# Optimization experiments

Measured on AMD Instinct MI355X. Metric: run time of the kernel, lower is better.

Reference implementation:

```python
import jax, jax.numpy as jnp
import numpy as np

B, C, T, V = 64, 3, 300, 25   # V == time_serious
CC, TS, TL = 100, 25, 9        # causal_channel, time_serious, time_len


def _bn2d(h, g, b, eps=1e-5):
    # training-mode BatchNorm2d: biased batch stats over (B, T, V)
    mu = h.mean(axis=(0, 2, 3), keepdims=True)
    var = h.var(axis=(0, 2, 3), keepdims=True)
    return g[None, :, None, None] * (h - mu) / jnp.sqrt(var + eps) + b[None, :, None, None]


def setup_inputs() -> dict:
    key = jax.random.key(0)
    ks = jax.random.split(key, 32)
    s = 0.1
    weight = jax.random.uniform(ks[1], (CC, TS, TL), minval=-0.163, maxval=0.163)  # ~kaiming_uniform fan_in=225
    inp = {
        'x': jax.random.normal(ks[0], (B, C, T, V)),
        'weight': weight,
        'weight_norm': jnp.linalg.norm(weight, axis=0),  # frozen at init, detached buffer
        'fb0_w': jax.random.normal(ks[2], (64, 3)) * s,
        'fb0_b': jax.random.normal(ks[3], (64,)) * s,
        'bn0_g': jnp.ones((64,)), 'bn0_b': jnp.zeros((64,)),
        'fb1_w': jax.random.normal(ks[4], (128, 64)) * s,
        'fb1_b': jax.random.normal(ks[5], (128,)) * s,
        'bn1_g': jnp.ones((128,)), 'bn1_b': jnp.zeros((128,)),
        'fb2_w': jax.random.normal(ks[6], (1, 128)) * s,
        'fb2_b': jax.random.normal(ks[7], (1,)) * s,
        'bn2_g': jnp.ones((1,)), 'bn2_b': jnp.zeros((1,)),
        'c1_w': jax.random.normal(ks[8], (CC, 1)) * s,
        'c1_b': jax.random.normal(ks[9], (CC,)) * s,
        'c2_w': jax.random.normal(ks[10], (CC, 1)) * s,
        'c2_b': jax.random.normal(ks[11], (CC,)) * s,
        'f0_w': jax.random.normal(ks[12], (TS, 100, 100)) * s,
        'f0_b': jax.random.normal(ks[13], (TS, 100)) * s,
        'f1_w': jax.random.normal(ks[14], (TS, 10, 100)) * s,
        'f1_b': jax.random.normal(ks[15], (TS, 10)) * s,
        'f2_w': jax.random.normal(ks[16], (TS, 1, 10)) * s,
        'f2_b': jax.random.normal(ks[17], (TS, 1)) * s,
    }
    return inp


def reference(x, weight, weight_norm, fb0_w, fb0_b, bn0_g, bn0_b, fb1_w, fb1_b, bn1_g, bn1_b,
              fb2_w, fb2_b, bn2_g, bn2_b, c1_w, c1_b, c2_w, c2_b,
              f0_w, f0_b, f1_w, f1_b, f2_w, f2_b):
    Bx, Cx, Tx, Vx = x.shape
    CCx, TSx, TLx = weight.shape
    L = Tx - TLx + 1

    # feature_update branches: 1x1 conv2d -> BN -> ReLU
    h = x
    for w, bb, g, bt in ((fb0_w, fb0_b, bn0_g, bn0_b),
                         (fb1_w, fb1_b, bn1_g, bn1_b),
                         (fb2_w, fb2_b, bn2_g, bn2_b)):
        h = jnp.einsum('oc,bctv->botv', w, h) + bb[None, :, None, None]
        h = jax.nn.relu(_bn2d(h, g, bt))
    # h: [B, 1, T, V]

    x1 = (jnp.einsum('oc,bctv->botv', c1_w, h) + c1_b[None, :, None, None]).mean(axis=2)  # [B,CC,V]
    x2 = (jnp.einsum('oc,bctv->botv', c2_w, h) + c2_b[None, :, None, None]).mean(axis=2)  # [B,CC,V]
    cm = jnp.tanh(x1[:, :, :, None] - x2[:, :, None, :])  # causal_matrix [B,CC,V,V]

    x_series = jnp.transpose(h[:, 0], (0, 2, 1))  # [B,V,T]
    wn = weight / jax.lax.stop_gradient(weight_norm)[None]  # [CC,TS,TL]

    # fused equivalent of the per-i grouped conv1d loop:
    # ret_i[b,c,t] = sum_{v,l} x_series[b,v,t+l] * cm[b,c,v,i] * wn[c,v,l]
    windows = jnp.stack([x_series[:, :, l:l + L] for l in range(TLx)], axis=-1)  # [B,V,L,TL]
    Fc = jnp.einsum('bvtl,cvl->bcvt', windows, wn)       # [B,CC,V,L]
    p = jnp.einsum('bcvi,bcvt->bict', cm, Fc)            # [B,TS,CC,L] (i = stacked channel group)

    # follow_branches: grouped 1x1 conv1d (groups = TS) + ReLU
    for w, bb in ((f0_w, f0_b), (f1_w, f1_b), (f2_w, f2_b)):
        p = jax.nn.relu(jnp.einsum('goc,bgct->bgot', w, p) + bb[None, :, :, None])
    p = p[:, :, 0, :]  # [B,V,L]

    predic_loss = jnp.mean((x_series[:, :, TLx:] - p[:, :, :-1]) ** 2)

    # GSGL penalty on causal_matrix
    n1 = jnp.linalg.norm(cm, axis=1)  # [B,V,V]
    panelty = 1e-4 * (jnp.linalg.norm(n1, axis=1).sum() + n1.sum())

    regularize = 1e-4 * (jnp.sum(f0_w ** 2) + jnp.sum(f1_w ** 2) + jnp.sum(f2_w ** 2))

    # GC: norm over channel then lag of cm[...,None] * weight -> closed form
    GCs = jnp.sqrt(jnp.einsum('bcvm,cm->bvm', cm ** 2, jnp.sum(weight ** 2, axis=-1)))
    return (GCs, predic_loss, panelty, regularize)
```

## Files before the change

kernel.cpp:

```cpp
#include <hip/hip_runtime.h>
#include <hip/hip_bf16.h>
#include <string.h>

#define N_POS 480000
#define NB    64
#define NT    300
#define NV    25
#define NCC   100
#define NTL   9
#define NL    292

#define WS_XA     0
#define WS_Z2SUM  144
#define WS_Z2SQ   160
#define WS_LOSS   176
#define WS_PAN    192
#define WS_REG    208
#define WS_SC1    224
#define WS_SH1    352
#define WS_SC2    480
#define WS_SH2    481
#define WS_WA     512
#define WS_W1T    768
#define WS_SW     8960
#define WS_HM     11460
#define WS_Z1P    13060
#define WS_Z1PQ   77060
#define WS_Z2     141060
#define WS_XS     621060
#define WS_CM     1101060
#define WS_P      5101060

__device__ __forceinline__ float waveRed(float v) {
    #pragma unroll
    for (int off = 32; off > 0; off >>= 1) v += __shfl_down(v, off);
    return v;
}

__global__ __launch_bounds__(256) void k_xstats(const float* __restrict__ x,
                                                float* __restrict__ ws) {
    __shared__ float s_red[4][9];
    int tid = blockIdx.x * 256 + threadIdx.x;
    int nth = gridDim.x * 256;
    float a[9];
    #pragma unroll
    for (int i = 0; i < 9; i++) a[i] = 0.f;
    for (int task = tid; task < 120000; task += nth) {
        int b = task / 1875; int q = task - b*1875;
        const float* xb = x + b*22500 + q*4;
        float4 v0 = *(const float4*)(xb);
        float4 v1 = *(const float4*)(xb + 7500);
        float4 v2 = *(const float4*)(xb + 15000);
        const float* p0 = (const float*)&v0;
        const float* p1 = (const float*)&v1;
        const float* p2 = (const float*)&v2;
        #pragma unroll
        for (int k = 0; k < 4; k++) {
            float x0 = p0[k], x1 = p1[k], x2 = p2[k];
            a[0] += x0; a[1] += x1; a[2] += x2;
            a[3] = fmaf(x0,x0,a[3]); a[4] = fmaf(x0,x1,a[4]); a[5] = fmaf(x0,x2,a[5]);
            a[6] = fmaf(x1,x1,a[6]); a[7] = fmaf(x1,x2,a[7]); a[8] = fmaf(x2,x2,a[8]);
        }
    }
    #pragma unroll
    for (int i = 0; i < 9; i++) a[i] = waveRed(a[i]);
    int w = threadIdx.x >> 6;
    if ((threadIdx.x & 63) == 0) {
        #pragma unroll
        for (int i = 0; i < 9; i++) s_red[w][i] = a[i];
    }
    __syncthreads();
    if (threadIdx.x < 9) {
        float s = s_red[0][threadIdx.x] + s_red[1][threadIdx.x]
                + s_red[2][threadIdx.x] + s_red[3][threadIdx.x];
        atomicAdd(&ws[WS_XA + threadIdx.x*16], s);
    }
}

__global__ void k_prepw(const float* __restrict__ weight, float* __restrict__ ws) {
    int idx = blockIdx.x * blockDim.x + threadIdx.x;
    if (idx < 2500) {
        float s = 0;
        #pragma unroll
        for (int l = 0; l < NTL; l++) { float w = weight[idx*NTL + l]; s += w*w; }
        ws[WS_SW + idx] = s;
    }
}

__global__ void k_prepw1t(const float* __restrict__ w1g, float* __restrict__ ws) {
    int idx = blockIdx.x * 256 + threadIdx.x;
    if (idx < 8192) {
        int c = idx >> 7, o = idx & 127;
        ws[WS_W1T + idx] = w1g[o*64 + c];
    }
}

__global__ void k_prep0(const float* __restrict__ w, const float* __restrict__ bb,
                        const float* __restrict__ g, const float* __restrict__ bt,
                        float* __restrict__ ws) {
    int o = threadIdx.x;
    float inv = 1.0f / (float)N_POS;
    float mx0 = ws[WS_XA+0]*inv, mx1 = ws[WS_XA+16]*inv, mx2 = ws[WS_XA+32]*inv;
    float C00 = ws[WS_XA+48]*inv  - mx0*mx0;
    float C01 = ws[WS_XA+64]*inv  - mx0*mx1;
    float C02 = ws[WS_XA+80]*inv  - mx0*mx2;
    float C11 = ws[WS_XA+96]*inv  - mx1*mx1;
    float C12 = ws[WS_XA+112]*inv - mx1*mx2;
    float C22 = ws[WS_XA+128]*inv - mx2*mx2;
    float w0 = w[o*3], w1 = w[o*3+1], w2 = w[o*3+2];
    float mu  = w0*mx0 + w1*mx1 + w2*mx2 + bb[o];
    float var = w0*w0*C00 + w1*w1*C11 + w2*w2*C22
              + 2.f*(w0*w1*C01 + w0*w2*C02 + w1*w2*C12);
    float sc = g[o] / sqrtf(var + 1e-5f);
    float sh = bt[o] - sc*mu;
    ws[WS_WA + o*4 + 0] = sc*w0;
    ws[WS_WA + o*4 + 1] = sc*w1;
    ws[WS_WA + o*4 + 2] = sc*w2;
    ws[WS_WA + o*4 + 3] = sc*bb[o] + sh;
}

#define ZP_BLOCKS 500
#define ZP_CHUNKS 15
template<int MODE>
__global__ __launch_bounds__(256) void k_zpass(
        const float* __restrict__ x,
        const float* __restrict__ b1g,
        const float* __restrict__ w2g,
        const float* __restrict__ b2g,
        float* __restrict__ ws) {
    __shared__ float smem[12544];
    float* s_h0  = smem;
    float* s_w1t = smem + 4352;
    int tid = threadIdx.x;

    for (int i = tid; i < 8192; i += 256) s_w1t[i] = ws[WS_W1T + i];

    int pos = tid & 63, cset = tid >> 6;
    int pg  = tid >> 4, og  = tid & 15;

    float b1r[8];
    #pragma unroll
    for (int o = 0; o < 8; o++) b1r[o] = b1g[og*8 + o];
    float sc1r[8], sh1r[8], w2r[8], b2v = 0.f;
    if constexpr (MODE == 1) {
        #pragma unroll
        for (int o = 0; o < 8; o++) {
            sc1r[o] = ws[WS_SC1 + og*8 + o];
            sh1r[o] = ws[WS_SH1 + og*8 + o];
            w2r[o]  = w2g[og*8 + o];
        }
        b2v = b2g[0];
    }
    float zs[8], zq[8];
    #pragma unroll
    for (int o = 0; o < 8; o++) { zs[o] = 0.f; zq[o] = 0.f; }
    float z2s = 0.f, z2q = 0.f;

    __syncthreads();

    for (int ci = 0; ci < ZP_CHUNKS; ci++) {
        int chunk = blockIdx.x * ZP_CHUNKS + ci;
        int P = chunk*64 + pos;
        int b = P / 7500, rem = P - b*7500;
        const float* xb = x + b*22500 + rem;
        float x0 = xb[0], x1 = xb[7500], x2 = xb[15000];
        #pragma unroll
        for (int k = 0; k < 16; k++) {
            int ch = cset*16 + k;
            const float4 wa = *(const float4*)&ws[WS_WA + ch*4];
            s_h0[ch*68 + pos] = fmaxf(wa.x*x0 + wa.y*x1 + wa.z*x2 + wa.w, 0.f);
        }
        __syncthreads();

        float acc[4][8];
        #pragma unroll
        for (int p = 0; p < 4; p++)
            #pragma unroll
            for (int o = 0; o < 8; o++) acc[p][o] = 0.f;

        #pragma unroll 4
        for (int c = 0; c < 64; c++) {
            float4 ha = *(const float4*)&s_h0[c*68 + 4*pg];
            float4 wl = *(const float4*)&s_w1t[c*128 + 8*og];
            float4 wh = *(const float4*)&s_w1t[c*128 + 8*og + 4];
            #pragma unroll
            for (int p = 0; p < 4; p++) {
                float hv = ((const float*)&ha)[p];
                #pragma unroll
                for (int o = 0; o < 4; o++) {
                    acc[p][o]   = fmaf(hv, ((const float*)&wl)[o], acc[p][o]);
                    acc[p][o+4] = fmaf(hv, ((const float*)&wh)[o], acc[p][o+4]);
                }
            }
        }

        if constexpr (MODE == 0) {
            #pragma unroll
            for (int o = 0; o < 8; o++) {
                #pragma unroll
                for (int p = 0; p < 4; p++) {
                    float z = acc[p][o] + b1r[o];
                    zs[o] += z; zq[o] += z*z;
                }
            }
            __syncthreads();
        } else {
            float zp[4];
            #pragma unroll
            for (int p = 0; p < 4; p++) {
                float s = 0.f;
                #pragma unroll
                for (int o = 0; o < 8; o++) {
                    float z = acc[p][o] + b1r[o];
                    s += w2r[o]*fmaxf(sc1r[o]*z + sh1r[o], 0.f);
                }
                zp[p] = s;
            }
            __syncthreads();
            float* s_z2p = smem;
            #pragma unroll
            for (int p = 0; p < 4; p++) s_z2p[(4*pg + p)*17 + og] = zp[p];
            __syncthreads();
            if (tid < 64) {
                float z2 = b2v;
                #pragma unroll
                for (int j = 0; j < 16; j++) z2 += s_z2p[tid*17 + j];
                ws[WS_Z2 + chunk*64 + tid] = z2;
                z2s += z2; z2q += z2*z2;
            }
            __syncthreads();
        }
    }

    if constexpr (MODE == 0) {
        float* s_part = smem;
        #pragma unroll
        for (int o = 0; o < 8; o++) s_part[(og*8 + o)*17 + pg] = zs[o];
        __syncthreads();
        if (tid < 128) {
            float s = 0.f;
            #pragma unroll
            for (int j = 0; j < 16; j++) s += s_part[tid*17 + j];
            ws[WS_Z1P + blockIdx.x*128 + tid] = s;
        }
        __syncthreads();
        #pragma unroll
        for (int o = 0; o < 8; o++) s_part[(og*8 + o)*17 + pg] = zq[o];
        __syncthreads();
        if (tid < 128) {
            float s = 0.f;
            #pragma unroll
            for (int j = 0; j < 16; j++) s += s_part[tid*17 + j];
            ws[WS_Z1PQ + blockIdx.x*128 + tid] = s;
        }
    } else {
        if (tid < 64) {
            z2s = waveRed(z2s);
            z2q = waveRed(z2q);
            if (tid == 0) { atomicAdd(&ws[WS_Z2SUM], z2s); atomicAdd(&ws[WS_Z2SQ], z2q); }
        }
    }
}

__global__ __launch_bounds__(256) void k_z1red(const float* __restrict__ g,
                                               const float* __restrict__ bt,
                                               float* __restrict__ ws) {
    __shared__ float ss[4], qq[4];
    int o = blockIdx.x;
    float s = 0.f, q = 0.f;
    for (int blk = threadIdx.x; blk < ZP_BLOCKS; blk += 256) {
        s += ws[WS_Z1P  + blk*128 + o];
        q += ws[WS_Z1PQ + blk*128 + o];
    }
    s = waveRed(s); q = waveRed(q);
    int w = threadIdx.x >> 6;
    if ((threadIdx.x & 63) == 0) { ss[w] = s; qq[w] = q; }
    __syncthreads();
    if (threadIdx.x == 0) {
        float S = ss[0]+ss[1]+ss[2]+ss[3];
        float Q = qq[0]+qq[1]+qq[2]+qq[3];
        float inv = 1.0f / (float)N_POS;
        float m = S*inv;
        float v = Q*inv - m*m;
        float sc = g[o] / sqrtf(v + 1e-5f);
        ws[WS_SC1+o] = sc;
        ws[WS_SH1+o] = bt[o] - sc*m;
    }
}

__global__ void k_prep2(const float* __restrict__ g, const float* __restrict__ bt,
                        float* __restrict__ ws) {
    float inv = 1.0f / (float)N_POS;
    float m = ws[WS_Z2SUM]*inv;
    float v = ws[WS_Z2SQ]*inv - m*m;
    float sc = g[0] / sqrtf(v + 1e-5f);
    ws[WS_SC2] = sc;
    ws[WS_SH2] = bt[0] - sc*m;
}

__global__ void k_xs(float* __restrict__ ws) {
    __shared__ float red[128];
    int bid = blockIdx.x;
    int b = bid / 25, v = bid - b*25;
    float sc = ws[WS_SC2], sh = ws[WS_SH2];
    float local = 0.f;
    for (int t = threadIdx.x; t < NT; t += 128) {
        float val = fmaxf(sc * ws[WS_Z2 + b*7500 + t*25 + v] + sh, 0.f);
        ws[WS_XS + (size_t)bid*NT + t] = val;
        local += val;
    }
    red[threadIdx.x] = local;
    __syncthreads();
    for (int s = 64; s > 0; s >>= 1) {
        if (threadIdx.x < s) red[threadIdx.x] += red[threadIdx.x + s];
        __syncthreads();
    }
    if (threadIdx.x == 0) ws[WS_HM + bid] = red[0] * (1.f/300.f);
}

__global__ void k_cm(const float* __restrict__ c1w, const float* __restrict__ c1b,
                     const float* __restrict__ c2w, const float* __restrict__ c2b,
                     float* __restrict__ ws) {
    __shared__ float s_hm[25];
    int bid = blockIdx.x;
    int b = bid / 100, c = bid - b*100;
    if (threadIdx.x < 25) s_hm[threadIdx.x] = ws[WS_HM + b*25 + threadIdx.x];
    float a1 = c1w[c], d1 = c1b[c], a2 = c2w[c], d2 = c2b[c];
    __syncthreads();
    for (int idx = threadIdx.x; idx < 625; idx += 256) {
        int i = idx / 25, j = idx - i*25;
        ws[WS_CM + (size_t)bid*625 + idx] = tanhf(a1*s_hm[i] + d1 - a2*s_hm[j] - d2);
    }
}

__global__ void k_gcs(const float* __restrict__ ws, float* __restrict__ out) {
    int gid = blockIdx.x * 256 + threadIdx.x;
    if (gid < 40000) {
        int b = gid / 625; int rem = gid - b*625; int m = rem % 25;
        float acc = 0.f;
        for (int c = 0; c < 100; c++) {
            float v = ws[WS_CM + ((size_t)(b*100+c))*625 + rem];
            acc += v*v*ws[WS_SW + c*25 + m];
        }
        out[gid] = sqrtf(acc);
    }
}

__global__ void k_pan(float* __restrict__ ws) {
    __shared__ float s_colsq[25];
    __shared__ float s_n1, s_r;
    int tid = threadIdx.x;
    int b = blockIdx.x;
    if (tid < 25) s_colsq[tid] = 0.f;
    if (tid == 0) { s_n1 = 0.f; s_r = 0.f; }
    __syncthreads();
    float ln1 = 0.f;
    for (int idx = tid; idx < 625; idx += 256) {
        int j = idx % 25;
        float sq = 0.f;
        for (int c = 0; c < 100; c++) {
            float v = ws[WS_CM + ((size_t)(b*100+c))*625 + idx];
            sq += v*v;
        }
        ln1 += sqrtf(sq);
        atomicAdd(&s_colsq[j], sq);
    }
    ln1 = waveRed(ln1);
    if ((tid & 63) == 0) atomicAdd(&s_n1, ln1);
    __syncthreads();
    if (tid < 25) atomicAdd(&s_r, sqrtf(s_colsq[tid]));
    __syncthreads();
    if (tid == 0) atomicAdd(&ws[WS_PAN], s_n1 + s_r);
}

__global__ void k_reg(const float* __restrict__ f0w, const float* __restrict__ f1w,
                      const float* __restrict__ f2w, float* __restrict__ ws) {
    __shared__ float sred[4];
    int tid = blockIdx.x * blockDim.x + threadIdx.x;
    int nth = gridDim.x * blockDim.x;
    float a = 0.f;
    for (int i = tid; i < 275250; i += nth) {
        float w;
        if (i < 250000) w = f0w[i];
        else if (i < 275000) w = f1w[i - 250000];
        else w = f2w[i - 275000];
        a += w*w;
    }
    a = waveRed(a);
    int w = threadIdx.x >> 6;
    if ((threadIdx.x & 63) == 0) sred[w] = a;
    __syncthreads();
    if (threadIdx.x == 0)
        atomicAdd(&ws[WS_REG], sred[0]+sred[1]+sred[2]+sred[3]);
}

#define XP 156
#define FP 152
__global__ __launch_bounds__(256) void k_fcp(
        const float* __restrict__ weight, const float* __restrict__ wnorm,
        float* __restrict__ pbuf, const float* __restrict__ ws, int b_base) {
    __shared__ float s_xs[25*XP];
    __shared__ float s_fc[25*FP];
    __shared__ float s_wn[225];
    __shared__ float s_cm[625];
    int tid = threadIdx.x;
    int bid = blockIdx.x;
    int bl = bid / 100, c = bid - bl*100;
    int b = b_base + bl;

    for (int i = tid; i < 225; i += 256) s_wn[i] = weight[c*225 + i] / wnorm[i];
    for (int i = tid; i < 625; i += 256) s_cm[i] = ws[WS_CM + ((size_t)(b*100+c))*625 + i];

    #pragma unroll
    for (int h = 0; h < 2; h++) {
        const int t_base = h ? 148 : 0;
        const int TH     = h ? 144 : 148;
        const int NTQ4   = TH / 4;
        const int NPV    = ((TH + 7) / 8);

        for (int i = tid; i < 25*XP; i += 256) {
            int v = i / XP, u = i - v*XP;
            if (u < TH + 8) s_xs[i] = ws[WS_XS + (size_t)(b*25+v)*NT + t_base + u];
        }
        __syncthreads();

        for (int task = tid; task < 25*NTQ4; task += 256) {
            int v = task / NTQ4, tq = task - v*NTQ4;
            int t0 = tq*4;
            float4 xa = *(const float4*)&s_xs[v*XP + t0];
            float4 xb = *(const float4*)&s_xs[v*XP + t0 + 4];
            float4 xc = *(const float4*)&s_xs[v*XP + t0 + 8];
            float xr[12];
            xr[0]=xa.x; xr[1]=xa.y; xr[2]=xa.z; xr[3]=xa.w;
            xr[4]=xb.x; xr[5]=xb.y; xr[6]=xb.z; xr[7]=xb.w;
            xr[8]=xc.x; xr[9]=xc.y; xr[10]=xc.z; xr[11]=xc.w;
            float f[4];
            #pragma unroll
            for (int k = 0; k < 4; k++) f[k] = 0.f;
            #pragma unroll
            for (int l = 0; l < NTL; l++) {
                float w = s_wn[v*NTL + l];
                #pragma unroll
                for (int k = 0; k < 4; k++) f[k] = fmaf(xr[k + l], w, f[k]);
            }
            *(float4*)&s_fc[v*FP + t0] = make_float4(f[0], f[1], f[2], f[3]);
        }
        __syncthreads();

        for (int task = tid; task < NPV*25; task += 256) {
            int tq = task / 25, ii = task - tq*25;
            int t0 = tq*8;
            float cmv[25];
            #pragma unroll
            for (int v = 0; v < 25; v++) cmv[v] = s_cm[v*25 + ii];
            float acc[8];
            #pragma unroll
            for (int k = 0; k < 8; k++) acc[k] = 0.f;
            #pragma unroll
            for (int v = 0; v < 25; v++) {
                float4 f0 = *(const float4*)&s_fc[v*FP + t0];
                float4 f1 = *(const float4*)&s_fc[v*FP + t0 + 4];
                float cv = cmv[v];
                acc[0] = fmaf(cv, f0.x, acc[0]);
                acc[1] = fmaf(cv, f0.y, acc[1]);
                acc[2] = fmaf(cv, f0.z, acc[2]);
                acc[3] = fmaf(cv, f0.w, acc[3]);
                acc[4] = fmaf(cv, f1.x, acc[4]);
                acc[5] = fmaf(cv, f1.y, acc[5]);
                acc[6] = fmaf(cv, f1.z, acc[6]);
                acc[7] = fmaf(cv, f1.w, acc[7]);
            }
            size_t row = (size_t)((bl*25 + ii)*100 + c);
            size_t gbase = row*NL + t_base + t0;
            *(float4*)(pbuf + gbase) = make_float4(acc[0], acc[1], acc[2], acc[3]);
            if (t0 + 8 <= TH)
                *(float4*)(pbuf + gbase + 4) = make_float4(acc[4], acc[5], acc[6], acc[7]);
        }
        __syncthreads();
    }
}

__global__ __launch_bounds__(256, 1) void k_mlp(
        const float* __restrict__ pbuf,
        const float* __restrict__ f0w, const float* __restrict__ f0b,
        const float* __restrict__ f1w, const float* __restrict__ f1b,
        const float* __restrict__ f2w, const float* __restrict__ f2b,
        float* __restrict__ ws, int b_base, int nb, int nchunks) {
    __shared__ float s_w1t[1000];
    __shared__ float s_loss;
    int tid = threadIdx.x;
    int g     = blockIdx.x / nchunks;
    int chunk = blockIdx.x - g*nchunks;
    for (int i = tid; i < 1000; i += 256) {
        int o = i / 10, o2 = i - o*10;
        s_w1t[i] = f1w[g*1000 + o2*100 + o];
    }
    if (tid == 0) s_loss = 0.f;
    __syncthreads();

    const float* w0 = f0w + g*10000;
    const float* b0 = f0b + g*100;
    const float* b1 = f1b + g*10;
    const float* w2 = f2w + g*10;
    float b2 = f2b[g];

    float local = 0.f;
    int tau = chunk*256 + tid;
    if (tau < nb*292) {
        int bl = tau / 292, t = tau - bl*292;
        const float* pg = pbuf + ((size_t)(bl*25 + g))*100*NL + t;
        float pr[100];
        #pragma unroll
        for (int cc = 0; cc < 100; cc++) pr[cc] = pg[(size_t)cc*NL];
        float acc2[10];
        #pragma unroll
        for (int o2 = 0; o2 < 10; o2++) acc2[o2] = b1[o2];
        for (int o = 0; o < 100; o += 2) {
            float a  = b0[o];
            float aa = b0[o+1];
            const float* wr  = w0 + o*100;
            const float* wr2 = wr + 100;
            #pragma unroll
            for (int cc = 0; cc < 100; cc++) {
                a  = fmaf(wr[cc],  pr[cc], a);
                aa = fmaf(wr2[cc], pr[cc], aa);
            }
            a  = fmaxf(a, 0.f);
            aa = fmaxf(aa, 0.f);
            #pragma unroll
            for (int o2 = 0; o2 < 10; o2++) {
                acc2[o2] = fmaf(s_w1t[o*10 + o2],     a,  acc2[o2]);
                acc2[o2] = fmaf(s_w1t[(o+1)*10 + o2], aa, acc2[o2]);
            }
        }
        float z3 = b2;
        #pragma unroll
        for (int o2 = 0; o2 < 10; o2++) z3 += w2[o2]*fmaxf(acc2[o2], 0.f);
        z3 = fmaxf(z3, 0.f);
        if (t < NL-1) {
            int b = b_base + bl;
            float d = ws[WS_XS + ((size_t)(b*25 + g))*NT + t + NTL] - z3;
            local = d*d;
        }
    }
    local = waveRed(local);
    if ((tid & 63) == 0) atomicAdd(&s_loss, local);
    __syncthreads();
    if (tid == 0) atomicAdd(&ws[WS_LOSS], s_loss);
}

__global__ void k_final(float* __restrict__ out, const float* __restrict__ ws) {
    out[40000] = ws[WS_LOSS] * (1.f / 465600.f);
    out[40001] = 1e-4f * ws[WS_PAN];
    out[40002] = 1e-4f * ws[WS_REG];
}

extern "C" void kernel_launch(void* const* d_in, const int* in_sizes, int n_in,
                              void* d_out, int out_size, void* d_ws, size_t ws_size,
                              hipStream_t stream) {
    const float* x      = (const float*)d_in[0];
    const float* weight = (const float*)d_in[1];
    const float* wnorm  = (const float*)d_in[2];
    const float* fb0_w  = (const float*)d_in[3];
    const float* fb0_b  = (const float*)d_in[4];
    const float* bn0_g  = (const float*)d_in[5];
    const float* bn0_b  = (const float*)d_in[6];
    const float* fb1_w  = (const float*)d_in[7];
    const float* fb1_b  = (const float*)d_in[8];
    const float* bn1_g  = (const float*)d_in[9];
    const float* bn1_b  = (const float*)d_in[10];
    const float* fb2_w  = (const float*)d_in[11];
    const float* fb2_b  = (const float*)d_in[12];
    const float* bn2_g  = (const float*)d_in[13];
    const float* bn2_b  = (const float*)d_in[14];
    const float* c1_w   = (const float*)d_in[15];
    const float* c1_b   = (const float*)d_in[16];
    const float* c2_w   = (const float*)d_in[17];
    const float* c2_b   = (const float*)d_in[18];
    const float* f0_w   = (const float*)d_in[19];
    const float* f0_b   = (const float*)d_in[20];
    const float* f1_w   = (const float*)d_in[21];
    const float* f1_b   = (const float*)d_in[22];
    const float* f2_w   = (const float*)d_in[23];
    const float* f2_b   = (const float*)d_in[24];

    float* ws  = (float*)d_ws;
    float* out = (float*)d_out;
    float* pbuf = ws + WS_P;

    hipMemsetAsync(d_ws, 0, 1024, stream);

    k_xstats<<<128, 256, 0, stream>>>(x, ws);
    k_prepw<<<10, 256, 0, stream>>>(weight, ws);
    k_prepw1t<<<32, 256, 0, stream>>>(fb1_w, ws);
    k_prep0<<<1, 64, 0, stream>>>(fb0_w, fb0_b, bn0_g, bn0_b, ws);
    k_zpass<0><<<ZP_BLOCKS, 256, 0, stream>>>(x, fb1_b, fb2_w, fb2_b, ws);
    k_z1red<<<128, 256, 0, stream>>>(bn1_g, bn1_b, ws);
    k_zpass<1><<<ZP_BLOCKS, 256, 0, stream>>>(x, fb1_b, fb2_w, fb2_b, ws);
    k_prep2<<<1, 1, 0, stream>>>(bn2_g, bn2_b, ws);
    k_xs<<<1600, 128, 0, stream>>>(ws);
    k_cm<<<6400, 256, 0, stream>>>(c1_w, c1_b, c2_w, c2_b, ws);
    k_gcs<<<157, 256, 0, stream>>>(ws, out);
    k_pan<<<64, 256, 0, stream>>>(ws);
    k_reg<<<256, 256, 0, stream>>>(f0_w, f1_w, f2_w, ws);

    const size_t p_bytes_per_b = (size_t)25*100*NL*sizeof(float);
    size_t fixed_bytes = (size_t)WS_P * sizeof(float);
    size_t avail = ws_size > fixed_bytes ? ws_size - fixed_bytes : 0;
    int bs = (int)(avail / p_bytes_per_b);
    if (bs > 64) bs = 64;
    if (bs < 1)  bs = 1;
    for (int b0 = 0; b0 < 64; b0 += bs) {
        int nb = (64 - b0) < bs ? (64 - b0) : bs;
        k_fcp<<<nb*100, 256, 0, stream>>>(weight, wnorm, pbuf, ws, b0);
        int nch = (nb*292 + 255) / 256;
        k_mlp<<<25*nch, 256, 0, stream>>>(pbuf, f0_w, f0_b, f1_w, f1_b,
                                          f2_w, f2_b, ws, b0, nb, nch);
    }
    k_final<<<1, 1, 0, stream>>>(out, ws);
}
```

Before: 754.9 us.

## Tile grouped MLP as shared-memory register-blocked GEMM with distributed loss reduction

```diff
diff --git a/kernel.cpp b/kernel.cpp
--- a/kernel.cpp
+++ b/kernel.cpp
@@ -480,79 +480,150 @@
     }
 }
 
-__global__ __launch_bounds__(256, 1) void k_mlp(
+__global__ __launch_bounds__(256) void k_mlp(
         const float* __restrict__ pbuf,
         const float* __restrict__ f0w, const float* __restrict__ f0b,
         const float* __restrict__ f1w, const float* __restrict__ f1b,
         const float* __restrict__ f2w, const float* __restrict__ f2b,
-        float* __restrict__ ws, int b_base, int nb, int nchunks) {
-    __shared__ float s_w1t[1000];
+        float* __restrict__ ws, int b_base) {
+    __shared__ float sm[11680];
     __shared__ float s_loss;
+    float* sP  = sm;
+    float* sW  = sm + 3536;
+    float* sW1 = sm + 10400;
     int tid = threadIdx.x;
-    int g     = blockIdx.x / nchunks;
-    int chunk = blockIdx.x - g*nchunks;
-    for (int i = tid; i < 1000; i += 256) {
-        int o = i / 10, o2 = i - o*10;
-        s_w1t[i] = f1w[g*1000 + o2*100 + o];
+    int bid = blockIdx.x;
+    int bl = bid / 125; int rem = bid - bl*125;
+    int g = rem / 5;    int tc = rem - g*5;
+    int t0 = tc*64;
+    int b = b_base + bl;
+    int og = tid & 15, pg = tid >> 4;
+
+    for (int i = tid; i < 1280; i += 256) {
+        int o2 = i >> 7, o = i & 127;
+        sW1[i] = (o < 100) ? f1w[g*1000 + o2*100 + o] : 0.f;
     }
     if (tid == 0) s_loss = 0.f;
-    __syncthreads();
-
-    const float* w0 = f0w + g*10000;
-    const float* b0 = f0b + g*100;
-    const float* b1 = f1b + g*10;
-    const float* w2 = f2w + g*10;
+
+    const float* Pbase = pbuf + (size_t)(bl*25 + g)*100*NL;
+    const float* W0 = f0w + g*10000;
+
+    float acc[4][8];
+    #pragma unroll
+    for (int p = 0; p < 4; p++)
+        #pragma unroll
+        for (int k = 0; k < 8; k++) acc[p][k] = 0.f;
+
+    #pragma unroll
+    for (int ch = 0; ch < 2; ch++) {
+        const int c0 = ch ? 52 : 0;
+        const int KL = ch ? 48 : 52;
+        const int NQ = KL / 4;
+        if (ch) __syncthreads();
+        for (int i = tid; i < KL*16; i += 256) {
+            int r = i >> 4, q = i & 15;
+            int t = t0 + 4*q;
+            float4 v = make_float4(0.f, 0.f, 0.f, 0.f);
+            if (t < NL) v = *(const float4*)(Pbase + (size_t)(c0 + r)*NL + t);
+            *(float4*)&sP[r*68 + 4*q] = v;
+        }
+        for (int i = tid; i < 100*NQ; i += 256) {
+            int o = i / NQ, q = i - o*NQ;
+            float4 v = *(const float4*)(W0 + o*100 + c0 + 4*q);
+            sW[(4*q+0)*132 + o] = v.x;
+            sW[(4*q+1)*132 + o] = v.y;
+            sW[(4*q+2)*132 + o] = v.z;
+            sW[(4*q+3)*132 + o] = v.w;
+        }
+        for (int i = tid; i < KL*28; i += 256) {
+            int r = i / 28, o = 100 + (i - r*28);
+            sW[r*132 + o] = 0.f;
+        }
+        __syncthreads();
+        #pragma unroll 4
+        for (int c = 0; c < KL; c++) {
+            float4 pv = *(const float4*)&sP[c*68 + 4*pg];
+            float4 wl = *(const float4*)&sW[c*132 + 8*og];
+            float4 wh = *(const float4*)&sW[c*132 + 8*og + 4];
+            #pragma unroll
+            for (int p = 0; p < 4; p++) {
+                float hv = ((const float*)&pv)[p];
+                #pragma unroll
+                for (int k = 0; k < 4; k++) {
+                    acc[p][k]   = fmaf(hv, ((const float*)&wl)[k], acc[p][k]);
+                    acc[p][k+4] = fmaf(hv, ((const float*)&wh)[k], acc[p][k+4]);
+                }
+            }
+        }
+    }
+
+    float b0r[8];
+    #pragma unroll
+    for (int k = 0; k < 8; k++) {
+        int o = og*8 + k;
+        b0r[k] = (o < 100) ? f0b[g*100 + o] : 0.f;
+    }
+    #pragma unroll
+    for (int p = 0; p < 4; p++)
+        #pragma unroll
+        for (int k = 0; k < 8; k++)
+            acc[p][k] = fmaxf(acc[p][k] + b0r[k], 0.f);
+
+    float acc2[4][10];
+    #pragma unroll
+    for (int o2 = 0; o2 < 10; o2++) {
+        float4 wA = *(const float4*)&sW1[o2*128 + og*8];
+        float4 wB = *(const float4*)&sW1[o2*128 + og*8 + 4];
+        #pragma unroll
+        for (int p = 0; p < 4; p++) {
+            float s;
+            s  = wA.x*acc[p][0]; s = fmaf(wA.y, acc[p][1], s);
+            s = fmaf(wA.z, acc[p][2], s); s = fmaf(wA.w, acc[p][3], s);
+            s = fmaf(wB.x, acc[p][4], s); s = fmaf(wB.y, acc[p][5], s);
+            s = fmaf(wB.z, acc[p][6], s); s = fmaf(wB.w, acc[p][7], s);
+            acc2[p][o2] = s;
+        }
+    }
+    #pragma unroll
+    for (int m = 1; m < 16; m <<= 1)
+        #pragma unroll
+        for (int p = 0; p < 4; p++)
+            #pragma unroll
+            for (int o2 = 0; o2 < 10; o2++)
+                acc2[p][o2] += __shfl_xor(acc2[p][o2], m);
+
+    float b1r[10], w2r[10];
+    #pragma unroll
+    for (int o2 = 0; o2 < 10; o2++) { b1r[o2] = f1b[g*10 + o2]; w2r[o2] = f2w[g*10 + o2]; }
     float b2 = f2b[g];
-
     float local = 0.f;
-    int tau = chunk*256 + tid;
-    if (tau < nb*292) {
-        int bl = tau / 292, t = tau - bl*292;
-        const float* pg = pbuf + ((size_t)(bl*25 + g))*100*NL + t;
-        float pr[100];
-        #pragma unroll
-        for (int cc = 0; cc < 100; cc++) pr[cc] = pg[(size_t)cc*NL];
-        float acc2[10];
-        #pragma unroll
-        for (int o2 = 0; o2 < 10; o2++) acc2[o2] = b1[o2];
-        for (int o = 0; o < 100; o += 2) {
-            float a  = b0[o];
-            float aa = b0[o+1];
-            const float* wr  = w0 + o*100;
-            const float* wr2 = wr + 100;
-            #pragma unroll
-            for (int cc = 0; cc < 100; cc++) {
-                a  = fmaf(wr[cc],  pr[cc], a);
-                aa = fmaf(wr2[cc], pr[cc], aa);
-            }
-            a  = fmaxf(a, 0.f);
-            aa = fmaxf(aa, 0.f);
-            #pragma unroll
-            for (int o2 = 0; o2 < 10; o2++) {
-                acc2[o2] = fmaf(s_w1t[o*10 + o2],     a,  acc2[o2]);
-                acc2[o2] = fmaf(s_w1t[(o+1)*10 + o2], aa, acc2[o2]);
-            }
-        }
-        float z3 = b2;
-        #pragma unroll
-        for (int o2 = 0; o2 < 10; o2++) z3 += w2[o2]*fmaxf(acc2[o2], 0.f);
-        z3 = fmaxf(z3, 0.f);
-        if (t < NL-1) {
-            int b = b_base + bl;
-            float d = ws[WS_XS + ((size_t)(b*25 + g))*NT + t + NTL] - z3;
-            local = d*d;
+    if (og == 0) {
+        #pragma unroll
+        for (int p = 0; p < 4; p++) {
+            int tg = t0 + 4*pg + p;
+            float z3 = b2;
+            #pragma unroll
+            for (int o2 = 0; o2 < 10; o2++)
+                z3 = fmaf(w2r[o2], fmaxf(acc2[p][o2] + b1r[o2], 0.f), z3);
+            z3 = fmaxf(z3, 0.f);
+            if (tg < NL-1) {
+                float d = ws[WS_XS + (size_t)(b*25 + g)*NT + tg + NTL] - z3;
+                local = fmaf(d, d, local);
+            }
         }
     }
     local = waveRed(local);
     if ((tid & 63) == 0) atomicAdd(&s_loss, local);
     __syncthreads();
-    if (tid == 0) atomicAdd(&ws[WS_LOSS], s_loss);
+    if (tid == 0) atomicAdd(&ws[WS_Z1P + (bid & 63)*16], s_loss);
 }
 
 __global__ void k_final(float* __restrict__ out, const float* __restrict__ ws) {
-    out[40000] = ws[WS_LOSS] * (1.f / 465600.f);
-    out[40001] = 1e-4f * ws[WS_PAN];
-    out[40002] = 1e-4f * ws[WS_REG];
+    float v = ws[WS_Z1P + threadIdx.x*16];
+    v = waveRed(v);
+    if (threadIdx.x == 0) out[40000] = v * (1.f / 465600.f);
+    if (threadIdx.x == 1) out[40001] = 1e-4f * ws[WS_PAN];
+    if (threadIdx.x == 2) out[40002] = 1e-4f * ws[WS_REG];
 }
 
 extern "C" void kernel_launch(void* const* d_in, const int* in_sizes, int n_in,
@@ -596,6 +667,7 @@
     k_prep0<<<1, 64, 0, stream>>>(fb0_w, fb0_b, bn0_g, bn0_b, ws);
     k_zpass<0><<<ZP_BLOCKS, 256, 0, stream>>>(x, fb1_b, fb2_w, fb2_b, ws);
     k_z1red<<<128, 256, 0, stream>>>(bn1_g, bn1_b, ws);
+    hipMemsetAsync((char*)d_ws + (size_t)WS_Z1P*4, 0, 64*16*4, stream);
     k_zpass<1><<<ZP_BLOCKS, 256, 0, stream>>>(x, fb1_b, fb2_w, fb2_b, ws);
     k_prep2<<<1, 1, 0, stream>>>(bn2_g, bn2_b, ws);
     k_xs<<<1600, 128, 0, stream>>>(ws);
@@ -613,9 +685,8 @@
     for (int b0 = 0; b0 < 64; b0 += bs) {
         int nb = (64 - b0) < bs ? (64 - b0) : bs;
         k_fcp<<<nb*100, 256, 0, stream>>>(weight, wnorm, pbuf, ws, b0);
-        int nch = (nb*292 + 255) / 256;
-        k_mlp<<<25*nch, 256, 0, stream>>>(pbuf, f0_w, f0_b, f1_w, f1_b,
-                                          f2_w, f2_b, ws, b0, nb, nch);
-    }
-    k_final<<<1, 1, 0, stream>>>(out, ws);
-}
+        k_mlp<<<nb*125, 256, 0, stream>>>(pbuf, f0_w, f0_b, f1_w, f1_b,
+                                          f2_w, f2_b, ws, b0);
+    }
+    k_final<<<1, 64, 0, stream>>>(out, ws);
+}
```

New measurement: 777.4 us. +3.0%, slower.

## Restructure MLP kernel to tile time in shared memory and split outputs across waves

Applied to the files above, without the earlier changes.

```diff
diff --git a/kernel.cpp b/kernel.cpp
--- a/kernel.cpp
+++ b/kernel.cpp
@@ -92,6 +92,15 @@
     if (idx < 8192) {
         int c = idx >> 7, o = idx & 127;
         ws[WS_W1T + idx] = w1g[o*64 + c];
+    }
+}
+
+__global__ void k_prepw0t(const float* __restrict__ f0w, float* __restrict__ w0t) {
+    int idx = blockIdx.x * 256 + threadIdx.x;
+    if (idx < 250000) {
+        int g = idx / 10000; int r = idx - g*10000;
+        int c = r / 100, o = r - c*100;
+        w0t[idx] = f0w[g*10000 + o*100 + c];
     }
 }
 
@@ -480,79 +489,100 @@
     }
 }
 
-__global__ __launch_bounds__(256, 1) void k_mlp(
-        const float* __restrict__ pbuf,
-        const float* __restrict__ f0w, const float* __restrict__ f0b,
+__global__ __launch_bounds__(256) void k_mlp(
+        const float* __restrict__ pbuf, const float* __restrict__ w0t,
+        const float* __restrict__ f0b,
         const float* __restrict__ f1w, const float* __restrict__ f1b,
         const float* __restrict__ f2w, const float* __restrict__ f2b,
-        float* __restrict__ ws, int b_base, int nb, int nchunks) {
-    __shared__ float s_w1t[1000];
-    __shared__ float s_loss;
+        float* __restrict__ ws, int b_base) {
+    __shared__ float sP[100*68];
     int tid = threadIdx.x;
-    int g     = blockIdx.x / nchunks;
-    int chunk = blockIdx.x - g*nchunks;
-    for (int i = tid; i < 1000; i += 256) {
-        int o = i / 10, o2 = i - o*10;
-        s_w1t[i] = f1w[g*1000 + o2*100 + o];
-    }
-    if (tid == 0) s_loss = 0.f;
-    __syncthreads();
-
-    const float* w0 = f0w + g*10000;
-    const float* b0 = f0b + g*100;
-    const float* b1 = f1b + g*10;
-    const float* w2 = f2w + g*10;
-    float b2 = f2b[g];
+    int bid = blockIdx.x;
+    int bl = bid / 125; int rem = bid - bl*125;
+    int g = rem / 5;    int tc = rem - g*5;
+    int t0 = tc*64;
+    int b = b_base + bl;
+    int lane = tid & 63;
+    int wv = __builtin_amdgcn_readfirstlane(tid >> 6);
+    int o_base = wv*25;
+
+    const float* Pg = pbuf + (size_t)(bl*25 + g)*100*NL;
+    for (int i = tid; i < 1600; i += 256) {
+        int r = i >> 4, q = i & 15;
+        int t = t0 + 4*q;
+        float4 v = make_float4(0.f, 0.f, 0.f, 0.f);
+        if (t + 3 < NL) {
+            v = *(const float4*)(Pg + (size_t)r*NL + t);
+        } else {
+            float tmp0 = (t+0 < NL) ? Pg[(size_t)r*NL + t+0] : 0.f;
+            float tmp1 = (t+1 < NL) ? Pg[(size_t)r*NL + t+1] : 0.f;
+            float tmp2 = (t+2 < NL) ? Pg[(size_t)r*NL + t+2] : 0.f;
+            float tmp3 = (t+3 < NL) ? Pg[(size_t)r*NL + t+3] : 0.f;
+            v = make_float4(tmp0, tmp1, tmp2, tmp3);
+        }
+        *(float4*)&sP[r*68 + 4*q] = v;
+    }
+    __syncthreads();
+
+    const float* w0g = w0t + g*10000;
+    float acc[25];
+    #pragma unroll
+    for (int k = 0; k < 25; k++) acc[k] = 0.f;
+    #pragma unroll 4
+    for (int c = 0; c < 100; c++) {
+        float pv = sP[c*68 + lane];
+        const float* wc = w0g + c*100 + o_base;
+        #pragma unroll
+        for (int k = 0; k < 25; k++)
+            acc[k] = fmaf(wc[k], pv, acc[k]);
+    }
+
+    float acc2[10];
+    #pragma unroll
+    for (int j = 0; j < 10; j++) acc2[j] = 0.f;
+    const float* b0g = f0b + g*100 + o_base;
+    const float* w1g = f1w + g*1000;
+    #pragma unroll
+    for (int k = 0; k < 25; k++) {
+        float h = fmaxf(acc[k] + b0g[k], 0.f);
+        #pragma unroll
+        for (int j = 0; j < 10; j++)
+            acc2[j] = fmaf(w1g[j*100 + o_base + k], h, acc2[j]);
+    }
+    __syncthreads();
+    float* s_red = sP;
+    #pragma unroll
+    for (int j = 0; j < 10; j++) s_red[(wv*10 + j)*68 + lane] = acc2[j];
+    __syncthreads();
 
     float local = 0.f;
-    int tau = chunk*256 + tid;
-    if (tau < nb*292) {
-        int bl = tau / 292, t = tau - bl*292;
-        const float* pg = pbuf + ((size_t)(bl*25 + g))*100*NL + t;
-        float pr[100];
-        #pragma unroll
-        for (int cc = 0; cc < 100; cc++) pr[cc] = pg[(size_t)cc*NL];
-        float acc2[10];
-        #pragma unroll
-        for (int o2 = 0; o2 < 10; o2++) acc2[o2] = b1[o2];
-        for (int o = 0; o < 100; o += 2) {
-            float a  = b0[o];
-            float aa = b0[o+1];
-            const float* wr  = w0 + o*100;
-            const float* wr2 = wr + 100;
-            #pragma unroll
-            for (int cc = 0; cc < 100; cc++) {
-                a  = fmaf(wr[cc],  pr[cc], a);
-                aa = fmaf(wr2[cc], pr[cc], aa);
-            }
-            a  = fmaxf(a, 0.f);
-            aa = fmaxf(aa, 0.f);
-            #pragma unroll
-            for (int o2 = 0; o2 < 10; o2++) {
-                acc2[o2] = fmaf(s_w1t[o*10 + o2],     a,  acc2[o2]);
-                acc2[o2] = fmaf(s_w1t[(o+1)*10 + o2], aa, acc2[o2]);
-            }
-        }
-        float z3 = b2;
-        #pragma unroll
-        for (int o2 = 0; o2 < 10; o2++) z3 += w2[o2]*fmaxf(acc2[o2], 0.f);
+    if (tid < 64) {
+        int tg = t0 + lane;
+        float z3 = f2b[g];
+        const float* b1g = f1b + g*10;
+        const float* w2g = f2w + g*10;
+        #pragma unroll
+        for (int j = 0; j < 10; j++) {
+            float s = s_red[j*68 + lane] + s_red[(10+j)*68 + lane]
+                    + s_red[(20+j)*68 + lane] + s_red[(30+j)*68 + lane];
+            z3 = fmaf(w2g[j], fmaxf(s + b1g[j], 0.f), z3);
+        }
         z3 = fmaxf(z3, 0.f);
-        if (t < NL-1) {
-            int b = b_base + bl;
-            float d = ws[WS_XS + ((size_t)(b*25 + g))*NT + t + NTL] - z3;
+        if (tg < NL-1) {
+            float d = ws[WS_XS + (size_t)(b*25 + g)*NT + tg + NTL] - z3;
             local = d*d;
         }
-    }
-    local = waveRed(local);
-    if ((tid & 63) == 0) atomicAdd(&s_loss, local);
-    __syncthreads();
-    if (tid == 0) atomicAdd(&ws[WS_LOSS], s_loss);
+        local = waveRed(local);
+        if (tid == 0) atomicAdd(&ws[WS_Z1P + (bid & 63)*16], local);
+    }
 }
 
 __global__ void k_final(float* __restrict__ out, const float* __restrict__ ws) {
-    out[40000] = ws[WS_LOSS] * (1.f / 465600.f);
-    out[40001] = 1e-4f * ws[WS_PAN];
-    out[40002] = 1e-4f * ws[WS_REG];
+    float v = ws[WS_Z1P + threadIdx.x*16];
+    v = waveRed(v);
+    if (threadIdx.x == 0) out[40000] = v * (1.f / 465600.f);
+    if (threadIdx.x == 1) out[40001] = 1e-4f * ws[WS_PAN];
+    if (threadIdx.x == 2) out[40002] = 1e-4f * ws[WS_REG];
 }
 
 extern "C" void kernel_launch(void* const* d_in, const int* in_sizes, int n_in,
@@ -586,16 +616,19 @@
 
     float* ws  = (float*)d_ws;
     float* out = (float*)d_out;
-    float* pbuf = ws + WS_P;
+    float* w0tp = ws + WS_P;
+    float* pbuf = ws + WS_P + 250000;
 
     hipMemsetAsync(d_ws, 0, 1024, stream);
 
     k_xstats<<<128, 256, 0, stream>>>(x, ws);
     k_prepw<<<10, 256, 0, stream>>>(weight, ws);
     k_prepw1t<<<32, 256, 0, stream>>>(fb1_w, ws);
+    k_prepw0t<<<977, 256, 0, stream>>>(f0_w, w0tp);
     k_prep0<<<1, 64, 0, stream>>>(fb0_w, fb0_b, bn0_g, bn0_b, ws);
     k_zpass<0><<<ZP_BLOCKS, 256, 0, stream>>>(x, fb1_b, fb2_w, fb2_b, ws);
     k_z1red<<<128, 256, 0, stream>>>(bn1_g, bn1_b, ws);
+    hipMemsetAsync((char*)d_ws + (size_t)WS_Z1P*4, 0, 64*16*4, stream);
     k_zpass<1><<<ZP_BLOCKS, 256, 0, stream>>>(x, fb1_b, fb2_w, fb2_b, ws);
     k_prep2<<<1, 1, 0, stream>>>(bn2_g, bn2_b, ws);
     k_xs<<<1600, 128, 0, stream>>>(ws);
@@ -605,7 +638,7 @@
     k_reg<<<256, 256, 0, stream>>>(f0_w, f1_w, f2_w, ws);
 
     const size_t p_bytes_per_b = (size_t)25*100*NL*sizeof(float);
-    size_t fixed_bytes = (size_t)WS_P * sizeof(float);
+    size_t fixed_bytes = (size_t)(WS_P + 250000) * sizeof(float);
     size_t avail = ws_size > fixed_bytes ? ws_size - fixed_bytes : 0;
     int bs = (int)(avail / p_bytes_per_b);
     if (bs > 64) bs = 64;
@@ -613,9 +646,8 @@
     for (int b0 = 0; b0 < 64; b0 += bs) {
         int nb = (64 - b0) < bs ? (64 - b0) : bs;
         k_fcp<<<nb*100, 256, 0, stream>>>(weight, wnorm, pbuf, ws, b0);
-        int nch = (nb*292 + 255) / 256;
-        k_mlp<<<25*nch, 256, 0, stream>>>(pbuf, f0_w, f0_b, f1_w, f1_b,
-                                          f2_w, f2_b, ws, b0, nb, nch);
-    }
-    k_final<<<1, 1, 0, stream>>>(out, ws);
-}
+        k_mlp<<<nb*125, 256, 0, stream>>>(pbuf, w0tp, f0_b, f1_w, f1_b,
+                                          f2_w, f2_b, ws, b0);
+    }
+    k_final<<<1, 64, 0, stream>>>(out, ws);
+}
```

Result: faster. 733.3 us (-2.9%).
